# Optimization experiments

Measured on AMD Instinct MI355X. Metric: run time of the kernel, lower is better.

The kernel has to match this reference:

```python
import jax, jax.numpy as jnp
import numpy as np

B, N, D = 32, 4096, 512
HID = 64
MIN_K, MAX_K = 3, 50
IN_DIM = 3 * D + 5  # mean/max/std pooled features + 5 structural features
NEG_SENTINEL = -1e8


def setup_inputs() -> dict:
    key = jax.random.key(0)
    ks = jax.random.split(key, 9)
    x = jax.random.normal(ks[0], (B, N, D), dtype=jnp.float32)
    keep = jax.random.uniform(ks[1], (B, 1, N)) < 0.75
    mask = jnp.where(keep, 0.0, -1e9).astype(jnp.float32)
    def lin(k, fan_in, fan_out):
        bound = 1.0 / np.sqrt(fan_in)
        kw, kb = jax.random.split(k)
        W = jax.random.uniform(kw, (fan_in, fan_out), minval=-bound, maxval=bound, dtype=jnp.float32)
        b = jax.random.uniform(kb, (fan_out,), minval=-bound, maxval=bound, dtype=jnp.float32)
        return W, b
    W1, b1 = lin(ks[2], IN_DIM, HID)
    W2, b2 = lin(ks[3], HID, HID // 2)
    W3, b3 = lin(ks[4], HID // 2, 1)
    return {"x": x, "mask": mask, "W1": W1, "b1": b1, "W2": W2, "b2": b2, "W3": W3, "b3": b3}


def reference(x, mask, W1, b1, W2, b2, W3, b3):
    valid = mask[:, 0, :] > NEG_SENTINEL            # [B, N] bool
    m = valid.astype(x.dtype)[..., None]            # [B, N, 1]
    cnt = m.sum(axis=1)                             # [B, 1] valid-node counts
    cnt_safe = jnp.maximum(cnt, 1.0)
    has_nodes = cnt > 0.0                           # [B, 1]

    # masked mean / max / unbiased std pooling (segment-reduce over nodes)
    x_mean = (x * m).sum(axis=1) / cnt_safe                                    # [B, D]
    x_mean = jnp.where(has_nodes, x_mean, 0.0)
    x_max = jnp.where(valid[..., None], x, -jnp.inf).max(axis=1)               # [B, D]
    x_max = jnp.where(has_nodes, x_max, 0.0)
    var = (m * (x - x_mean[:, None, :]) ** 2).sum(axis=1) / jnp.maximum(cnt - 1.0, 1.0)
    x_std = jnp.where(has_nodes, jnp.sqrt(var), 0.0)                           # [B, D]

    # structural features: dense path with no edge_index -> constants except log_size
    n = cnt[:, 0]
    log_size = jnp.log(n + 1.0) / 5.0
    ones = jnp.ones_like(log_size)
    # [log_size, density=0.1, avg_degree/10=0.2, max_degree=4.0, degree_std/10=0.1]
    sf = jnp.stack([log_size, 0.1 * ones, 0.2 * ones, 4.0 * ones, 0.1 * ones], axis=1)  # [B, 5]

    g = jnp.concatenate([x_mean, x_max, x_std, sf], axis=1)   # [B, 3D+5]
    h = jax.nn.relu(g @ W1 + b1)                              # dropout is identity in eval
    h = jax.nn.relu(h @ W2 + b2)
    score = jax.nn.sigmoid(h @ W3 + b3)[:, 0]                 # [B]

    num_clusters_cont = MIN_K + score * (MAX_K - MIN_K)
    num_clusters = jnp.round(num_clusters_cont).mean().astype(jnp.int32)
    num_clusters = jnp.clip(num_clusters, MIN_K, MAX_K)
    return num_clusters, score.mean()
```

## Files before the change

kernel.cpp:

```cpp
#include <hip/hip_runtime.h>
#include <cmath>

#define B_      32
#define N_      4096
#define D_      512
#define D4      (D_/4)
#define NCH     64
#define RPC     64
#define IN_DIM  1541
#define NEG_SENT (-1.0e8f)
#define BIGNEG   (1.0e30f)

__global__ __launch_bounds__(128) void stats_partial_kernel(
    const float* __restrict__ x, const float* __restrict__ mask,
    float4* __restrict__ psum, float4* __restrict__ psq,
    float4* __restrict__ pmax, float* __restrict__ pcnt)
{
    __shared__ float sw[RPC];
    __shared__ float so[RPC];
    const int tx = threadIdx.x;
    const int c  = blockIdx.x;
    const int b  = blockIdx.y;

    if (tx < RPC) {
        const float mv = mask[b * N_ + c * RPC + tx];
        const float w  = (mv > NEG_SENT) ? 1.f : 0.f;
        sw[tx] = w;
        so[tx] = (w - 1.f) * BIGNEG;
        float cv = w;
        #pragma unroll
        for (int off = 32; off > 0; off >>= 1) cv += __shfl_down(cv, off);
        if (tx == 0) pcnt[b * NCH + c] = cv;
    }
    __syncthreads();

    const float4* __restrict__ xb =
        (const float4*)x + ((size_t)b * N_ + (size_t)c * RPC) * D4 + tx;

    float4 s  = {0,0,0,0};
    float4 q  = {0,0,0,0};
    float4 mx = {-BIGNEG,-BIGNEG,-BIGNEG,-BIGNEG};

    #pragma unroll 4
    for (int j = 0; j < RPC; ++j) {
        const float4 v = xb[(size_t)j * D4];
        const float  w = sw[j];
        const float  o = so[j];
        const float tvx = v.x*w, tvy = v.y*w, tvz = v.z*w, tvw = v.w*w;
        s.x += tvx; s.y += tvy; s.z += tvz; s.w += tvw;
        q.x = fmaf(tvx, v.x, q.x); q.y = fmaf(tvy, v.y, q.y);
        q.z = fmaf(tvz, v.z, q.z); q.w = fmaf(tvw, v.w, q.w);
        mx.x = fmaxf(mx.x, fmaf(w, v.x, o));
        mx.y = fmaxf(mx.y, fmaf(w, v.y, o));
        mx.z = fmaxf(mx.z, fmaf(w, v.z, o));
        mx.w = fmaxf(mx.w, fmaf(w, v.w, o));
    }

    const size_t idx = ((size_t)(b * NCH + c)) * D4 + tx;
    psum[idx] = s; psq[idx] = q; pmax[idx] = mx;
}

__global__ __launch_bounds__(256) void mlp_kernel(
    const float4* __restrict__ psum, const float4* __restrict__ psq,
    const float4* __restrict__ pmax, const float* __restrict__ pcnt,
    const float* __restrict__ W1, const float* __restrict__ b1,
    const float* __restrict__ W2, const float* __restrict__ b2,
    const float* __restrict__ W3, const float* __restrict__ b3,
    float* __restrict__ scores)
{
    __shared__ float4 Ss[2][D4], Sq[2][D4], Sm[2][D4];
    __shared__ float g[IN_DIM];
    __shared__ float h1p[4*64];
    __shared__ float h1[64];
    __shared__ float h2[32];
    __shared__ float scnt;

    const int tid = threadIdx.x;
    const int tx  = tid & 127;
    const int ty  = tid >> 7;
    const int b   = blockIdx.x;

    {
        float4 s = {0,0,0,0}, q = {0,0,0,0};
        float4 mx = {-BIGNEG,-BIGNEG,-BIGNEG,-BIGNEG};
        const int c0 = ty * (NCH/2);
        #pragma unroll 4
        for (int c = c0; c < c0 + NCH/2; ++c) {
            const size_t idx = ((size_t)(b * NCH + c)) * D4 + tx;
            float4 a = psum[idx], u = psq[idx], w = pmax[idx];
            s.x += a.x; s.y += a.y; s.z += a.z; s.w += a.w;
            q.x += u.x; q.y += u.y; q.z += u.z; q.w += u.w;
            mx.x = fmaxf(mx.x,w.x); mx.y = fmaxf(mx.y,w.y);
            mx.z = fmaxf(mx.z,w.z); mx.w = fmaxf(mx.w,w.w);
        }
        Ss[ty][tx] = s; Sq[ty][tx] = q; Sm[ty][tx] = mx;
    }
    if (tid < 64) {
        float cv = pcnt[b * NCH + tid];
        #pragma unroll
        for (int off = 32; off > 0; off >>= 1) cv += __shfl_down(cv, off);
        if (tid == 0) scnt = cv;
    }
    __syncthreads();

    const float cnt = scnt;
    if (ty == 0) {
        float4 s = Ss[0][tx], s_ = Ss[1][tx];
        float4 q = Sq[0][tx], q_ = Sq[1][tx];
        float4 mx = Sm[0][tx], m_ = Sm[1][tx];
        s.x += s_.x; s.y += s_.y; s.z += s_.z; s.w += s_.w;
        q.x += q_.x; q.y += q_.y; q.z += q_.z; q.w += q_.w;
        mx.x = fmaxf(mx.x,m_.x); mx.y = fmaxf(mx.y,m_.y);
        mx.z = fmaxf(mx.z,m_.z); mx.w = fmaxf(mx.w,m_.w);

        const bool  has = cnt > 0.f;
        const float inv = 1.f / fmaxf(cnt, 1.f);
        const float dn  = 1.f / fmaxf(cnt - 1.f, 1.f);
        float sa[4] = {s.x,s.y,s.z,s.w};
        float qa[4] = {q.x,q.y,q.z,q.w};
        float ma[4] = {mx.x,mx.y,mx.z,mx.w};
        #pragma unroll
        for (int k = 0; k < 4; ++k) {
            const int d = 4*tx + k;
            const float mn = has ? sa[k] * inv : 0.f;
            const float vv = fmaxf((qa[k] - cnt * mn * mn) * dn, 0.f);
            g[d]        = mn;
            g[D_ + d]   = has ? ma[k] : 0.f;
            g[2*D_ + d] = has ? sqrtf(vv) : 0.f;
        }
        if (tx == 0) {
            g[3*D_ + 0] = logf(cnt + 1.f) * 0.2f;
            g[3*D_ + 1] = 0.1f;
            g[3*D_ + 2] = 0.2f;
            g[3*D_ + 3] = 4.0f;
            g[3*D_ + 4] = 0.1f;
        }
    }
    __syncthreads();

    {
        const int o   = tid & 63;
        const int grp = tid >> 6;
        float a = 0.f;
        #pragma unroll 4
        for (int i = grp; i < IN_DIM; i += 4)
            a = fmaf(g[i], W1[i*64 + o], a);
        h1p[tid] = a;
    }
    __syncthreads();
    if (tid < 64) {
        float a = b1[tid] + ((h1p[tid] + h1p[64+tid]) + (h1p[128+tid] + h1p[192+tid]));
        h1[tid] = fmaxf(a, 0.f);
    }
    __syncthreads();

    if (tid < 32) {
        float a = b2[tid];
        #pragma unroll
        for (int i = 0; i < 64; ++i) a = fmaf(h1[i], W2[i*32 + tid], a);
        h2[tid] = fmaxf(a, 0.f);
    }
    __syncthreads();

    if (tid == 0) {
        float a = b3[0];
        #pragma unroll
        for (int i = 0; i < 32; ++i) a = fmaf(h2[i], W3[i], a);
        scores[b] = 1.f / (1.f + expf(-a));
    }
}

__global__ __launch_bounds__(64) void final_kernel(
    const float* __restrict__ scores, float* __restrict__ out)
{
    const int t = threadIdx.x;
    float sc = (t < B_) ? scores[t] : 0.f;
    float r  = (t < B_) ? rintf(3.f + sc * 47.f) : 0.f;
    #pragma unroll
    for (int off = 32; off > 0; off >>= 1) {
        sc += __shfl_down(sc, off);
        r  += __shfl_down(r,  off);
    }
    if (t == 0) {
        const float mean_r = r * (1.f / 32.f);
        int nc = (int)mean_r;
        nc = nc < 3 ? 3 : (nc > 50 ? 50 : nc);
        out[0] = (float)nc;
        out[1] = sc * (1.f / 32.f);
    }
}

extern "C" void kernel_launch(void* const* d_in, const int* in_sizes, int n_in,
                              void* d_out, int out_size, void* d_ws, size_t ws_size,
                              hipStream_t stream)
{
    const float* x    = (const float*)d_in[0];
    const float* mask = (const float*)d_in[1];
    const float* W1   = (const float*)d_in[2];
    const float* b1   = (const float*)d_in[3];
    const float* W2   = (const float*)d_in[4];
    const float* b2   = (const float*)d_in[5];
    const float* W3   = (const float*)d_in[6];
    const float* b3   = (const float*)d_in[7];
    float* out = (float*)d_out;

    const size_t PCOUNT = (size_t)B_ * NCH * D4;
    float4* psum = (float4*)d_ws;
    float4* psq  = psum + PCOUNT;
    float4* pmax = psq  + PCOUNT;
    float*  pcnt = (float*)(pmax + PCOUNT);
    float*  scores = pcnt + (size_t)B_ * NCH;

    dim3 gridA(NCH, B_);
    stats_partial_kernel<<<gridA, 128, 0, stream>>>(x, mask, psum, psq, pmax, pcnt);
    mlp_kernel<<<B_, 256, 0, stream>>>(psum, psq, pmax, pcnt,
                                       W1, b1, W2, b2, W3, b3, scores);
    final_kernel<<<1, 64, 0, stream>>>(scores, out);
}
```

Before: 420.7 us.

## Split MLP into combine, split-K layer1, and single-block finish kernels

New measurement: 397.1 us. -5.6%, faster.

```diff
diff --git a/kernel.cpp b/kernel.cpp
--- a/kernel.cpp
+++ b/kernel.cpp
@@ -8,6 +8,9 @@
 #define NCH     64
 #define RPC     64
 #define IN_DIM  1541
+#define GSTRIDE 1568
+#define NSPLIT  8
+#define CHUNK   193
 #define NEG_SENT (-1.0e8f)
 #define BIGNEG   (1.0e30f)
 
@@ -60,19 +63,12 @@
     psum[idx] = s; psq[idx] = q; pmax[idx] = mx;
 }
 
-__global__ __launch_bounds__(256) void mlp_kernel(
+__global__ __launch_bounds__(256) void combine_g_kernel(
     const float4* __restrict__ psum, const float4* __restrict__ psq,
     const float4* __restrict__ pmax, const float* __restrict__ pcnt,
-    const float* __restrict__ W1, const float* __restrict__ b1,
-    const float* __restrict__ W2, const float* __restrict__ b2,
-    const float* __restrict__ W3, const float* __restrict__ b3,
-    float* __restrict__ scores)
+    float* __restrict__ g_all)
 {
     __shared__ float4 Ss[2][D4], Sq[2][D4], Sm[2][D4];
-    __shared__ float g[IN_DIM];
-    __shared__ float h1p[4*64];
-    __shared__ float h1[64];
-    __shared__ float h2[32];
     __shared__ float scnt;
 
     const int tid = threadIdx.x;
@@ -104,6 +100,7 @@
     __syncthreads();
 
     const float cnt = scnt;
+    float* __restrict__ g = g_all + (size_t)b * GSTRIDE;
     if (ty == 0) {
         float4 s = Ss[0][tx], s_ = Ss[1][tx];
         float4 q = Sq[0][tx], q_ = Sq[1][tx];
@@ -136,57 +133,79 @@
             g[3*D_ + 4] = 0.1f;
         }
     }
+}
+
+__global__ __launch_bounds__(64) void layer1_kernel(
+    const float* __restrict__ g_all, const float* __restrict__ W1,
+    float* __restrict__ h1p)
+{
+    __shared__ float sg[CHUNK];
+    const int o  = threadIdx.x;
+    const int c  = blockIdx.x;
+    const int b  = blockIdx.y;
+    const int i0 = c * CHUNK;
+    const int len = (IN_DIM - i0) < CHUNK ? (IN_DIM - i0) : CHUNK;
+
+    for (int j = o; j < len; j += 64) sg[j] = g_all[(size_t)b * GSTRIDE + i0 + j];
+    __syncthreads();
+
+    const float* __restrict__ Wp = W1 + (size_t)i0 * 64 + o;
+    float a = 0.f;
+    #pragma unroll 8
+    for (int k = 0; k < len; ++k)
+        a = fmaf(sg[k], Wp[(size_t)k * 64], a);
+    h1p[((size_t)b * NSPLIT + c) * 64 + o] = a;
+}
+
+__global__ __launch_bounds__(1024) void finish_kernel(
+    const float* __restrict__ h1p, const float* __restrict__ b1,
+    const float* __restrict__ W2, const float* __restrict__ b2,
+    const float* __restrict__ W3, const float* __restrict__ b3,
+    float* __restrict__ out)
+{
+    __shared__ float h1s[B_ * 64];
+    __shared__ float h2s[B_ * 33];
+    const int tid = threadIdx.x;
+
+    #pragma unroll
+    for (int r = 0; r < 2; ++r) {
+        const int oi = tid + r * 1024;
+        const int b = oi >> 6, o = oi & 63;
+        float a = b1[o];
+        #pragma unroll
+        for (int c = 0; c < NSPLIT; ++c) a += h1p[((size_t)b * NSPLIT + c) * 64 + o];
+        h1s[oi] = fmaxf(a, 0.f);
+    }
     __syncthreads();
 
     {
-        const int o   = tid & 63;
-        const int grp = tid >> 6;
-        float a = 0.f;
-        #pragma unroll 4
-        for (int i = grp; i < IN_DIM; i += 4)
-            a = fmaf(g[i], W1[i*64 + o], a);
-        h1p[tid] = a;
-    }
-    __syncthreads();
-    if (tid < 64) {
-        float a = b1[tid] + ((h1p[tid] + h1p[64+tid]) + (h1p[128+tid] + h1p[192+tid]));
-        h1[tid] = fmaxf(a, 0.f);
+        const int b = tid >> 5, o = tid & 31;
+        float a = b2[o];
+        #pragma unroll
+        for (int i = 0; i < 64; ++i) a = fmaf(h1s[b*64 + i], W2[i*32 + o], a);
+        h2s[b*33 + o] = fmaxf(a, 0.f);
     }
     __syncthreads();
 
     if (tid < 32) {
-        float a = b2[tid];
-        #pragma unroll
-        for (int i = 0; i < 64; ++i) a = fmaf(h1[i], W2[i*32 + tid], a);
-        h2[tid] = fmaxf(a, 0.f);
-    }
-    __syncthreads();
-
-    if (tid == 0) {
+        const int b = tid;
         float a = b3[0];
         #pragma unroll
-        for (int i = 0; i < 32; ++i) a = fmaf(h2[i], W3[i], a);
-        scores[b] = 1.f / (1.f + expf(-a));
-    }
-}
-
-__global__ __launch_bounds__(64) void final_kernel(
-    const float* __restrict__ scores, float* __restrict__ out)
-{
-    const int t = threadIdx.x;
-    float sc = (t < B_) ? scores[t] : 0.f;
-    float r  = (t < B_) ? rintf(3.f + sc * 47.f) : 0.f;
-    #pragma unroll
-    for (int off = 32; off > 0; off >>= 1) {
-        sc += __shfl_down(sc, off);
-        r  += __shfl_down(r,  off);
-    }
-    if (t == 0) {
-        const float mean_r = r * (1.f / 32.f);
-        int nc = (int)mean_r;
-        nc = nc < 3 ? 3 : (nc > 50 ? 50 : nc);
-        out[0] = (float)nc;
-        out[1] = sc * (1.f / 32.f);
+        for (int i = 0; i < 32; ++i) a = fmaf(h2s[b*33 + i], W3[i], a);
+        float sc = 1.f / (1.f + expf(-a));
+        float r  = rintf(3.f + sc * 47.f);
+        #pragma unroll
+        for (int off = 16; off > 0; off >>= 1) {
+            sc += __shfl_down(sc, off);
+            r  += __shfl_down(r,  off);
+        }
+        if (tid == 0) {
+            const float mean_r = r * (1.f / 32.f);
+            int nc = (int)mean_r;
+            nc = nc < 3 ? 3 : (nc > 50 ? 50 : nc);
+            out[0] = (float)nc;
+            out[1] = sc * (1.f / 32.f);
+        }
     }
 }
 
@@ -209,11 +228,13 @@
     float4* psq  = psum + PCOUNT;
     float4* pmax = psq  + PCOUNT;
     float*  pcnt = (float*)(pmax + PCOUNT);
-    float*  scores = pcnt + (size_t)B_ * NCH;
+    float*  g_all = pcnt + (size_t)B_ * NCH;
+    float*  h1p   = g_all + (size_t)B_ * GSTRIDE;
 
     dim3 gridA(NCH, B_);
     stats_partial_kernel<<<gridA, 128, 0, stream>>>(x, mask, psum, psq, pmax, pcnt);
-    mlp_kernel<<<B_, 256, 0, stream>>>(psum, psq, pmax, pcnt,
-                                       W1, b1, W2, b2, W3, b3, scores);
-    final_kernel<<<1, 64, 0, stream>>>(scores, out);
-}
+    combine_g_kernel<<<B_, 256, 0, stream>>>(psum, psq, pmax, pcnt, g_all);
+    dim3 gridL1(NSPLIT, B_);
+    layer1_kernel<<<gridL1, 64, 0, stream>>>(g_all, W1, h1p);
+    finish_kernel<<<1, 1024, 0, stream>>>(h1p, b1, W2, b2, W3, b3, out);
+}
```
